# Performance work log

Measured on AMD Instinct MI355X. Metric: run time of the kernel, lower is better.

The kernel has to match this reference:

```python
import jax, jax.numpy as jnp
import numpy as np

HIDDEN = 384
NDIM = 3
N_POINTS = 100000
N_SUPER = 2048
MAX_DEG = 32
RADIUS = 0.045
INPUT_DIM = 3


def _sincos_embed(coords):
    # ContinuousSincosEmbed: dim=384, ndim=3 -> 128 channels per spatial dim (64 sin + 64 cos)
    eff = HIDDEN // NDIM  # 128
    omega = jnp.arange(0, eff, 2, dtype=jnp.float32) / eff
    freq = 1.0 / (10000.0 ** omega)  # [eff//2]
    out = coords[..., None] * freq  # [..., ndim, eff//2]
    emb = jnp.concatenate([jnp.sin(out), jnp.cos(out)], axis=-1)  # [..., ndim, eff]
    return emb.reshape(coords.shape[:-1] + (HIDDEN,))


def _radius_neighbors(pos, sn_idx):
    # numpy preprocessing equivalent of torch_geometric.nn.pool.radius with
    # max_num_neighbors=MAX_DEG; fixed-size padded [S, K] output + validity mask.
    nbr = np.zeros((N_SUPER, MAX_DEG), np.int32)
    mask = np.zeros((N_SUPER, MAX_DEG), bool)
    pos2 = (pos ** 2).sum(-1)
    r2 = RADIUS * RADIUS
    chunk = 128
    for i0 in range(0, N_SUPER, chunk):
        sp = pos[sn_idx[i0:i0 + chunk]]
        d2 = (sp ** 2).sum(-1)[:, None] + pos2[None, :] - 2.0 * (sp @ pos.T)
        within = d2 <= r2
        for j in range(sp.shape[0]):
            idx = np.nonzero(within[j])[0][:MAX_DEG]
            nbr[i0 + j, :len(idx)] = idx
            mask[i0 + j, :len(idx)] = True
    return nbr, mask


def setup_inputs() -> dict:
    rng = np.random.default_rng(0)
    pos = rng.random((N_POINTS, NDIM)).astype(np.float32)
    sn_idx = np.sort(rng.choice(N_POINTS, N_SUPER, replace=False)).astype(np.int32)
    nbr, mask = _radius_neighbors(pos, sn_idx)
    key = jax.random.key(0)
    ks = jax.random.split(key, 6)
    s = 0.02  # truncnormal002 init scale
    return {
        "input_pos": jnp.asarray(pos),
        "input_feat": jax.random.normal(ks[0], (N_POINTS, INPUT_DIM), jnp.float32),
        "supernode_idx": jnp.asarray(sn_idx),
        "neighbor_idx": jnp.asarray(nbr),
        "neighbor_mask": jnp.asarray(mask),
        "W_in": jax.random.normal(ks[1], (INPUT_DIM, HIDDEN), jnp.float32) * s,
        "b_in": jnp.zeros((HIDDEN,), jnp.float32),
        "W1": jax.random.normal(ks[2], (2 * HIDDEN, HIDDEN), jnp.float32) * s,
        "b1": jnp.zeros((HIDDEN,), jnp.float32),
        "W2": jax.random.normal(ks[3], (HIDDEN, HIDDEN), jnp.float32) * s,
        "b2": jnp.zeros((HIDDEN,), jnp.float32),
        "W_proj": jax.random.normal(ks[4], (2 * HIDDEN, HIDDEN), jnp.float32) * s,
        "b_proj": jnp.zeros((HIDDEN,), jnp.float32),
    }


def reference(input_pos, input_feat, supernode_idx, neighbor_idx, neighbor_mask,
              W_in, b_in, W1, b1, W2, b2, W_proj, b_proj):
    # point embeddings: continuous sincos pos embed + input feature projection
    x = _sincos_embed(input_pos) + input_feat @ W_in + b_in          # [N, D]
    sn = x[supernode_idx]                                            # [S, D] supernode pos embed
    src = x[neighbor_idx]                                            # [S, K, D] gathered neighbors
    dst = jnp.broadcast_to(sn[:, None, :], src.shape)                # [S, K, D]
    h = jnp.concatenate([src, dst], axis=-1)                         # [S, K, 2D]
    # message MLP (Linear -> GELU(exact) -> Linear), as nn.GELU default
    h = jax.nn.gelu(h @ W1 + b1, approximate=False) @ W2 + b2        # [S, K, D]
    # masked mean == segment_csr(..., reduce='mean') over variable-degree edges
    m = neighbor_mask[..., None].astype(h.dtype)
    agg = (h * m).sum(axis=1) / jnp.maximum(m.sum(axis=1), 1.0)      # [S, D]
    # readd_supernode_pos: concat supernode pos embed, project 2D -> D
    out = jnp.concatenate([agg, sn], axis=-1) @ W_proj + b_proj      # [S, D]
    return out[None]                                                 # [1, S, D] (batch_size=1)
```

## Files before the change

### kernel.cpp

```cpp
#include <hip/hip_runtime.h>
#include <hip/hip_bf16.h>
#include <cstdint>

#define HIDDEN 384
#define NSUPER 2048
#define FRAGS (12*24*64)
#define WBLK  (FRAGS*8)

typedef __attribute__((ext_vector_type(8))) short bf16x8;
typedef __attribute__((ext_vector_type(4))) float f32x4;

__device__ inline unsigned short f2bf(float f) {
    unsigned int u = __float_as_uint(f);
    return (unsigned short)((u + 0x7fffu + ((u >> 16) & 1u)) >> 16);
}
__device__ inline bf16x8 pack8(const float* v) {
    union { bf16x8 v8; unsigned short u[8]; } u;
    #pragma unroll
    for (int i = 0; i < 8; ++i) u.u[i] = f2bf(v[i]);
    return u.v8;
}
__device__ inline float gelu(float y) {
    const float y2 = y * y;
    const float m  = __expf(y * fmaf(-0.0713548163f, y2, -1.5957691216f));
    return y * (1.0f / (1.0f + m));
}

__global__ __launch_bounds__(256)
void prep(const float* __restrict__ W1, const float* __restrict__ W2,
          const float* __restrict__ Wp, const unsigned int* __restrict__ mask,
          const float* __restrict__ pos, const float* __restrict__ feat,
          const int* __restrict__ sn_idx,
          const float* __restrict__ W_in, const float* __restrict__ b_in,
          unsigned short* __restrict__ w1sf, unsigned short* __restrict__ w1df,
          unsigned short* __restrict__ w2f,  unsigned short* __restrict__ wpf,
          unsigned short* __restrict__ snxb, int* __restrict__ flag) {
    const int b = blockIdx.x;
    const int t = threadIdx.x;
    if (b == 360) {
        __shared__ int s;
        if (t == 0) s = 0;
        __syncthreads();
        int bad = 0;
        for (int i = t; i < 16384; i += 256)
            if (mask[i] > 1u) bad = 1;
        if (bad) s = 1;
        __syncthreads();
        if (t == 0) *flag = s;
        return;
    }
    if (b > 360) {
        __shared__ float W4[HIDDEN][4];
        __shared__ float P6[64][7];
        const int eb = b - 361;
        if (t < 64) {
            const int pi = sn_idx[eb*64 + t];
            P6[t][0]=pos[pi*3];  P6[t][1]=pos[pi*3+1];  P6[t][2]=pos[pi*3+2];
            P6[t][3]=feat[pi*3]; P6[t][4]=feat[pi*3+1]; P6[t][5]=feat[pi*3+2];
        }
        for (int d = t; d < HIDDEN; d += 256) {
            W4[d][0]=W_in[d]; W4[d][1]=W_in[HIDDEN+d];
            W4[d][2]=W_in[2*HIDDEN+d]; W4[d][3]=b_in[d];
        }
        __syncthreads();
        const int er = t >> 2, seg = t & 3;
        float frA[8], frB[8];
        #pragma unroll
        for (int i = 0; i < 8; ++i) {
            frA[i] = exp2f(-(float)(seg*8 + i)      * 0.2076205059304601f);
            frB[i] = exp2f(-(float)(32 + seg*8 + i) * 0.2076205059304601f);
        }
        const float f0 = P6[er][3], f1 = P6[er][4], f2 = P6[er][5];
        #pragma unroll
        for (int cc = 0; cc < 3; ++cc) {
            const float pc = P6[er][cc];
            float sL[8], sH[8], cL[8], cH[8];
            #pragma unroll
            for (int i = 0; i < 8; ++i) {
                const float aL = pc*frA[i], aH = pc*frB[i];
                sL[i]=__sinf(aL); sH[i]=__sinf(aH); cL[i]=__cosf(aL); cH[i]=__cosf(aH);
            }
            #pragma unroll
            for (int q = 0; q < 4; ++q) {
                const float* bb = (q==0)?sL:(q==1)?sH:(q==2)?cL:cH;
                const int blk = cc*4 + q;
                float v[8];
                #pragma unroll
                for (int i = 0; i < 8; ++i) {
                    const int dim = blk*32 + seg*8 + i;
                    const float4 wv = *(const float4*)W4[dim];
                    v[i] = fmaf(f0, wv.x, fmaf(f1, wv.y, fmaf(f2, wv.z, bb[i] + wv.w)));
                }
                *(bf16x8*)&snxb[(size_t)(eb*64 + er)*HIDDEN + blk*32 + seg*8] = pack8(v);
            }
        }
        return;
    }
    const int grp = b / 72, sub = b % 72;
    const float* W; unsigned short* out;
    switch (grp) {
        case 0: W = W1;              out = w1sf; break;
        case 1: W = W1 + 384*HIDDEN; out = w1df; break;
        case 2: W = W2;              out = w2f;  break;
        case 3: W = Wp;              out = wpf;  break;
        default:W = Wp + 384*HIDDEN; out = wpf + WBLK; break;
    }
    const int idx = sub * 256 + t;
    const int l   = idx & 63;
    const int frag= idx >> 6;
    const int nt  = frag % 24;
    const int kt  = frag / 24;
    const int col = nt * 16 + (l & 15);
    const int k0  = kt * 32 + (l >> 4) * 8;
    unsigned int pk[4];
    #pragma unroll
    for (int j = 0; j < 4; ++j) {
        unsigned int lo = f2bf(W[(size_t)(k0 + 2*j)     * HIDDEN + col]);
        unsigned int hi = f2bf(W[(size_t)(k0 + 2*j + 1) * HIDDEN + col]);
        pk[j] = lo | (hi << 16);
    }
    *reinterpret_cast<uint4*>(&out[(size_t)idx * 8]) =
        *reinterpret_cast<const uint4*>(pk);
}

__global__ __launch_bounds__(256)
void k_dstv(const unsigned short* __restrict__ snxb,
            const unsigned short* __restrict__ w1df,
            const float* __restrict__ b1, float* __restrict__ dstv) {
    const int rg = blockIdx.x >> 2, cq = blockIdx.x & 3;
    const int t = threadIdx.x, w = t>>6, l = t&63, lg = l>>4, l15 = l&15;
    const int wgm = w>>1, wgn = w&1;
    const int r0 = rg*64 + wgm*32;
    const int ntb = cq*6 + wgn*3;
    f32x4 acc[2][3];
    #pragma unroll
    for (int mt=0; mt<2; ++mt)
        #pragma unroll
        for (int nt=0; nt<3; ++nt) acc[mt][nt] = (f32x4){0.f,0.f,0.f,0.f};
    #pragma unroll 2
    for (int kt = 0; kt < 12; ++kt) {
        bf16x8 a[2], bfr[3];
        const unsigned short* bpp = &w1df[((size_t)(kt*24 + ntb)*64 + l)*8];
        #pragma unroll
        for (int nt=0; nt<3; ++nt) bfr[nt] = *(const bf16x8*)(bpp + (size_t)nt*512);
        #pragma unroll
        for (int mt=0; mt<2; ++mt)
            a[mt] = *(const bf16x8*)&snxb[(size_t)(r0 + mt*16 + l15)*HIDDEN + kt*32 + lg*8];
        #pragma unroll
        for (int mt=0; mt<2; ++mt)
            #pragma unroll
            for (int nt=0; nt<3; ++nt)
                acc[mt][nt] = __builtin_amdgcn_mfma_f32_16x16x32_bf16(a[mt], bfr[nt], acc[mt][nt], 0,0,0);
    }
    #pragma unroll
    for (int mt=0; mt<2; ++mt)
        #pragma unroll
        for (int nt=0; nt<3; ++nt) {
            const int col = cq*96 + wgn*48 + nt*16 + l15;
            #pragma unroll
            for (int r=0; r<4; ++r) {
                const int row = r0 + mt*16 + lg*4 + r;
                dstv[(size_t)row*HIDDEN + col] = acc[mt][nt][r] + b1[col];
            }
        }
}

__global__ __launch_bounds__(512, 2)
void k_mlp(const float* __restrict__ pos, const float* __restrict__ feat,
           const int* __restrict__ nbr_idx, const void* __restrict__ mask_raw,
           const int* __restrict__ mask_fmt,
           const float* __restrict__ W_in, const float* __restrict__ b_in,
           const float* __restrict__ dstv,
           const unsigned short* __restrict__ W1sf,
           unsigned short* __restrict__ aggpre, float* __restrict__ cntf)
{
    __shared__ unsigned short G[8*12*64*8];
    __shared__ ushort4 WINTB[HIDDEN];
    __shared__ float PF[128][7];
    __shared__ float CNT[4];

    const int t  = threadIdx.x;
    const int bm = blockIdx.x;
    const int l = t & 63, w = t >> 6;
    const int mg = w >> 2, ng = w & 3;
    const int lg = l >> 4, l15 = l & 15;

    float dvreg[2][6];
    #pragma unroll
    for (int sl = 0; sl < 2; ++sl)
        #pragma unroll
        for (int nt = 0; nt < 6; ++nt)
            dvreg[sl][nt] = dstv[(size_t)(bm*4 + mg*2 + sl)*HIDDEN + ng*96 + nt*16 + l15];

    if (t < 128) {
        const int e  = bm*128 + t;
        const int pi = nbr_idx[e];
        PF[t][0]=pos[pi*3];  PF[t][1]=pos[pi*3+1];  PF[t][2]=pos[pi*3+2];
        PF[t][3]=feat[pi*3]; PF[t][4]=feat[pi*3+1]; PF[t][5]=feat[pi*3+2];
        const int fmt = *mask_fmt;
        const int mv  = fmt ? (int)((const unsigned char*)mask_raw)[e]
                            : ((const int*)mask_raw)[e];
        PF[t][6] = mv ? 1.0f : 0.0f;
    }
    if (t >= 128 && t < 128 + HIDDEN) {
        const int d = t - 128;
        ushort4 wv;
        wv.x = f2bf(W_in[d]); wv.y = f2bf(W_in[HIDDEN+d]);
        wv.z = f2bf(W_in[2*HIDDEN+d]); wv.w = f2bf(b_in[d]);
        WINTB[d] = wv;
    }
    __syncthreads();
    if (t < 4) {
        float c = 0.f;
        for (int s = 0; s < 32; ++s) c += PF[t*32+s][6];
        CNT[t] = c;
    }

    {
        const int er = t >> 2, seg = t & 3;
        float frA[8], frB[8];
        #pragma unroll
        for (int i = 0; i < 8; ++i) {
            frA[i] = exp2f(-(float)(seg*8 + i)      * 0.2076205059304601f);
            frB[i] = exp2f(-(float)(32 + seg*8 + i) * 0.2076205059304601f);
        }
        const float f0 = PF[er][3], f1 = PF[er][4], f2 = PF[er][5];
        const float pc0 = PF[er][0], pc1 = PF[er][1], pc2 = PF[er][2];
        const int slotbase = (er>>4)*12*64 + seg*16 + (er&15);
        #pragma unroll
        for (int kt = 0; kt < 12; ++kt) {
            const float pc = (kt>>2)==0 ? pc0 : ((kt>>2)==1 ? pc1 : pc2);
            float v[8];
            #pragma unroll
            for (int i = 0; i < 8; ++i) {
                const float fr = (kt&1) ? frB[i] : frA[i];
                const float aa = pc * fr;
                const float base = ((kt>>1)&1) ? __cosf(aa) : __sinf(aa);
                const ushort4 wv = WINTB[kt*32 + seg*8 + i];
                v[i] = fmaf(__uint_as_float((unsigned)wv.x<<16), f0,
                       fmaf(__uint_as_float((unsigned)wv.y<<16), f1,
                       fmaf(__uint_as_float((unsigned)wv.z<<16), f2,
                            base + __uint_as_float((unsigned)wv.w<<16))));
            }
            *(bf16x8*)&G[(size_t)(slotbase + kt*64)*8] = pack8(v);
        }
    }
    __syncthreads();

    f32x4 acc[4][6];
    #pragma unroll
    for (int mt=0; mt<4; ++mt)
        #pragma unroll
        for (int nt=0; nt<6; ++nt) acc[mt][nt] = (f32x4){0.f,0.f,0.f,0.f};

    bf16x8 bA[6], bB[6];
    #define LOADB(dst, kt)                                                      \
        { const unsigned short* bp_ = &W1sf[((size_t)((kt)*24 + ng*6)*64 + l)*8];\
          _Pragma("unroll")                                                     \
          for (int nt_ = 0; nt_ < 6; ++nt_)                                     \
              dst[nt_] = *(const bf16x8*)(bp_ + (size_t)nt_*512); }
    #define AREAD(a_, kt)                                                       \
        { _Pragma("unroll")                                                     \
          for (int mt_ = 0; mt_ < 4; ++mt_)                                     \
              a_[mt_] = *(const bf16x8*)&G[(size_t)((((mg*4 + mt_)*12 + (kt))*64) + l)*8]; }
    #define MFMA6(bfr, a_)                                                      \
        { __builtin_amdgcn_s_setprio(1);                                        \
          _Pragma("unroll")                                                     \
          for (int mt_ = 0; mt_ < 4; ++mt_)                                     \
              _Pragma("unroll")                                                 \
              for (int nt_ = 0; nt_ < 6; ++nt_)                                 \
                  acc[mt_][nt_] = __builtin_amdgcn_mfma_f32_16x16x32_bf16(      \
                      a_[mt_], bfr[nt_], acc[mt_][nt_], 0, 0, 0);               \
          __builtin_amdgcn_s_setprio(0); }

    LOADB(bA, 0); LOADB(bB, 1);
    #pragma unroll
    for (int kt = 0; kt < 12; kt += 2) {
        bf16x8 a[4];
        AREAD(a, kt);
        MFMA6(bA, a);
        if (kt + 2 < 12) LOADB(bA, kt + 2);
        AREAD(a, kt + 1);
        MFMA6(bB, a);
        if (kt + 3 < 12) LOADB(bB, kt + 3);
    }

    float mvr[4][4];
    #pragma unroll
    for (int mt=0; mt<4; ++mt)
        #pragma unroll
        for (int r=0; r<4; ++r)
            mvr[mt][r] = PF[(mg*4 + mt)*16 + lg*4 + r][6];
    #pragma unroll
    for (int nt=0; nt<6; ++nt) {
        const int col = ng*96 + nt*16 + l15;
        float s0 = 0.f, s1 = 0.f;
        #pragma unroll
        for (int mt=0; mt<4; ++mt) {
            const float dv = dvreg[mt>>1][nt];
            float p = 0.f;
            #pragma unroll
            for (int r=0; r<4; ++r)
                p += mvr[mt][r] * gelu(acc[mt][nt][r] + dv);
            if (mt < 2) s0 += p; else s1 += p;
        }
        s0 += __shfl_xor(s0,16); s0 += __shfl_xor(s0,32);
        s1 += __shfl_xor(s1,16); s1 += __shfl_xor(s1,32);
        if (lg == 0) {
            const int sn0 = bm*4 + mg*2;
            aggpre[(size_t)sn0*HIDDEN + col]     = f2bf(s0 / fmaxf(CNT[mg*2],1.f));
            aggpre[(size_t)(sn0+1)*HIDDEN + col] = f2bf(s1 / fmaxf(CNT[mg*2+1],1.f));
        }
    }
    if (t < 4) cntf[bm*4 + t] = CNT[t];
    #undef LOADB
    #undef AREAD
    #undef MFMA6
}

__global__ __launch_bounds__(256)
void k_agg(const unsigned short* __restrict__ aggpre,
           const unsigned short* __restrict__ w2f,
           const float* __restrict__ b2, const float* __restrict__ cntf,
           unsigned short* __restrict__ aggb) {
    const int rg = blockIdx.x >> 2, cq = blockIdx.x & 3;
    const int t = threadIdx.x, w = t>>6, l = t&63, lg = l>>4, l15 = l&15;
    const int wgm = w>>1, wgn = w&1;
    const int r0 = rg*64 + wgm*32;
    const int ntb = cq*6 + wgn*3;
    f32x4 acc[2][3];
    #pragma unroll
    for (int mt=0; mt<2; ++mt)
        #pragma unroll
        for (int nt=0; nt<3; ++nt) acc[mt][nt] = (f32x4){0.f,0.f,0.f,0.f};
    #pragma unroll 2
    for (int kt = 0; kt < 12; ++kt) {
        bf16x8 a[2], bfr[3];
        const unsigned short* bpp = &w2f[((size_t)(kt*24 + ntb)*64 + l)*8];
        #pragma unroll
        for (int nt=0; nt<3; ++nt) bfr[nt] = *(const bf16x8*)(bpp + (size_t)nt*512);
        #pragma unroll
        for (int mt=0; mt<2; ++mt)
            a[mt] = *(const bf16x8*)&aggpre[(size_t)(r0 + mt*16 + l15)*HIDDEN + kt*32 + lg*8];
        #pragma unroll
        for (int mt=0; mt<2; ++mt)
            #pragma unroll
            for (int nt=0; nt<3; ++nt)
                acc[mt][nt] = __builtin_amdgcn_mfma_f32_16x16x32_bf16(a[mt], bfr[nt], acc[mt][nt], 0,0,0);
    }
    #pragma unroll
    for (int mt=0; mt<2; ++mt)
        #pragma unroll
        for (int nt=0; nt<3; ++nt) {
            const int col = cq*96 + wgn*48 + nt*16 + l15;
            const float bb = b2[col];
            #pragma unroll
            for (int r=0; r<4; ++r) {
                const int row = r0 + mt*16 + lg*4 + r;
                const float nz = (cntf[row] > 0.f) ? 1.f : 0.f;
                aggb[(size_t)row*HIDDEN + col] = f2bf(acc[mt][nt][r] + bb*nz);
            }
        }
}

__global__ __launch_bounds__(256)
void k_proj(const unsigned short* __restrict__ aggb,
            const unsigned short* __restrict__ snxb,
            const unsigned short* __restrict__ wpf,
            const float* __restrict__ bp, float* __restrict__ out) {
    const int rg = blockIdx.x >> 2, cq = blockIdx.x & 3;
    const int t = threadIdx.x, w = t>>6, l = t&63, lg = l>>4, l15 = l&15;
    const int wgm = w>>1, wgn = w&1;
    const int r0 = rg*64 + wgm*32;
    const int ntb = cq*6 + wgn*3;
    f32x4 acc[2][3];
    #pragma unroll
    for (int mt=0; mt<2; ++mt)
        #pragma unroll
        for (int nt=0; nt<3; ++nt) acc[mt][nt] = (f32x4){0.f,0.f,0.f,0.f};
    #pragma unroll 2
    for (int kt = 0; kt < 24; ++kt) {
        const unsigned short* Ab = (kt < 12) ? aggb : snxb;
        const unsigned short* Wb = (kt < 12) ? wpf  : wpf + WBLK;
        const int ktt = (kt < 12) ? kt : kt - 12;
        bf16x8 a[2], bfr[3];
        const unsigned short* bpp = &Wb[((size_t)(ktt*24 + ntb)*64 + l)*8];
        #pragma unroll
        for (int nt=0; nt<3; ++nt) bfr[nt] = *(const bf16x8*)(bpp + (size_t)nt*512);
        #pragma unroll
        for (int mt=0; mt<2; ++mt)
            a[mt] = *(const bf16x8*)&Ab[(size_t)(r0 + mt*16 + l15)*HIDDEN + ktt*32 + lg*8];
        #pragma unroll
        for (int mt=0; mt<2; ++mt)
            #pragma unroll
            for (int nt=0; nt<3; ++nt)
                acc[mt][nt] = __builtin_amdgcn_mfma_f32_16x16x32_bf16(a[mt], bfr[nt], acc[mt][nt], 0,0,0);
    }
    #pragma unroll
    for (int mt=0; mt<2; ++mt)
        #pragma unroll
        for (int nt=0; nt<3; ++nt) {
            const int col = cq*96 + wgn*48 + nt*16 + l15;
            #pragma unroll
            for (int r=0; r<4; ++r) {
                const int row = r0 + mt*16 + lg*4 + r;
                out[(size_t)row*HIDDEN + col] = acc[mt][nt][r] + bp[col];
            }
        }
}

extern "C" void kernel_launch(void* const* d_in, const int* in_sizes, int n_in,
                              void* d_out, int out_size, void* d_ws, size_t ws_size,
                              hipStream_t stream) {
    const float* pos   = (const float*)d_in[0];
    const float* feat  = (const float*)d_in[1];
    const int*   sn    = (const int*)d_in[2];
    const int*   nbr   = (const int*)d_in[3];
    const void*  mask  = d_in[4];
    const float* W_in  = (const float*)d_in[5];
    const float* b_in  = (const float*)d_in[6];
    const float* W1    = (const float*)d_in[7];
    const float* b1    = (const float*)d_in[8];
    const float* W2    = (const float*)d_in[9];
    const float* b2    = (const float*)d_in[10];
    const float* Wp    = (const float*)d_in[11];
    const float* bpv   = (const float*)d_in[12];
    float* out = (float*)d_out;

    char* base = (char*)d_ws;
    int* flag = (int*)base;
    unsigned short* w1sf = (unsigned short*)(base + 256);
    unsigned short* w1df = w1sf + WBLK;
    unsigned short* w2f  = w1df + WBLK;
    unsigned short* wpf  = w2f  + WBLK;
    unsigned short* snxb = wpf  + 2*(size_t)WBLK;
    unsigned short* aggb = snxb + (size_t)NSUPER*HIDDEN;
    unsigned short* aggp = aggb + (size_t)NSUPER*HIDDEN;
    float* cntf = (float*)(aggp + (size_t)NSUPER*HIDDEN);
    float* dstv = cntf + NSUPER;

    hipLaunchKernelGGL(prep, dim3(393), dim3(256), 0, stream,
                       W1, W2, Wp, (const unsigned int*)mask,
                       pos, feat, sn, W_in, b_in,
                       w1sf, w1df, w2f, wpf, snxb, flag);
    hipLaunchKernelGGL(k_dstv, dim3(128), dim3(256), 0, stream,
                       snxb, w1df, b1, dstv);
    hipLaunchKernelGGL(k_mlp, dim3(512), dim3(512), 0, stream,
                       pos, feat, nbr, mask, flag, W_in, b_in, dstv,
                       w1sf, aggp, cntf);
    hipLaunchKernelGGL(k_agg, dim3(128), dim3(256), 0, stream,
                       aggp, w2f, b2, cntf, aggb);
    hipLaunchKernelGGL(k_proj, dim3(128), dim3(256), 0, stream,
                       aggb, snxb, wpf, bpv, out);
}
```

Measured before the change: 87.21 us.

## Fuse W2 aggregation GEMM into projection kernel via shared-memory tile

Merges the k_agg and k_proj kernels into one k_out kernel. Each block computes the full 64x384 W2 output for its row group into shared memory, then runs the projection GEMM from that tile, removing one launch and the aggb global round trip. In exchange, each of the four column-quarter blocks per row group recomputes the whole W2 GEMM (4x redundant work), and the accumulator array per wave grows to 24 tiles, which raises register pressure. Separately, the input-projection weights in k_mlp are now kept as fp32 float4 in shared memory instead of bf16-packed values.

```diff
diff --git a/kernel.cpp b/kernel.cpp
--- a/kernel.cpp
+++ b/kernel.cpp
@@ -175,7 +175,7 @@
            unsigned short* __restrict__ aggpre, float* __restrict__ cntf)
 {
     __shared__ unsigned short G[8*12*64*8];
-    __shared__ ushort4 WINTB[HIDDEN];
+    __shared__ float4 WINT[HIDDEN];
     __shared__ float PF[128][7];
     __shared__ float CNT[4];
 
@@ -204,10 +204,7 @@
     }
     if (t >= 128 && t < 128 + HIDDEN) {
         const int d = t - 128;
-        ushort4 wv;
-        wv.x = f2bf(W_in[d]); wv.y = f2bf(W_in[HIDDEN+d]);
-        wv.z = f2bf(W_in[2*HIDDEN+d]); wv.w = f2bf(b_in[d]);
-        WINTB[d] = wv;
+        WINT[d] = (float4){W_in[d], W_in[HIDDEN+d], W_in[2*HIDDEN+d], b_in[d]};
     }
     __syncthreads();
     if (t < 4) {
@@ -236,11 +233,8 @@
                 const float fr = (kt&1) ? frB[i] : frA[i];
                 const float aa = pc * fr;
                 const float base = ((kt>>1)&1) ? __cosf(aa) : __sinf(aa);
-                const ushort4 wv = WINTB[kt*32 + seg*8 + i];
-                v[i] = fmaf(__uint_as_float((unsigned)wv.x<<16), f0,
-                       fmaf(__uint_as_float((unsigned)wv.y<<16), f1,
-                       fmaf(__uint_as_float((unsigned)wv.z<<16), f2,
-                            base + __uint_as_float((unsigned)wv.w<<16))));
+                const float4 wv = WINT[kt*32 + seg*8 + i];
+                v[i] = fmaf(f0, wv.x, fmaf(f1, wv.y, fmaf(f2, wv.z, base + wv.w)));
             }
             *(bf16x8*)&G[(size_t)(slotbase + kt*64)*8] = pack8(v);
         }
@@ -319,59 +313,56 @@
 }
 
 __global__ __launch_bounds__(256)
-void k_agg(const unsigned short* __restrict__ aggpre,
+void k_out(const unsigned short* __restrict__ aggpre,
+           const unsigned short* __restrict__ snxb,
            const unsigned short* __restrict__ w2f,
-           const float* __restrict__ b2, const float* __restrict__ cntf,
-           unsigned short* __restrict__ aggb) {
+           const unsigned short* __restrict__ wpf,
+           const float* __restrict__ b2, const float* __restrict__ bp,
+           const float* __restrict__ cntf, float* __restrict__ out) {
+    __shared__ unsigned short AGG[64][392];
     const int rg = blockIdx.x >> 2, cq = blockIdx.x & 3;
     const int t = threadIdx.x, w = t>>6, l = t&63, lg = l>>4, l15 = l&15;
     const int wgm = w>>1, wgn = w&1;
-    const int r0 = rg*64 + wgm*32;
-    const int ntb = cq*6 + wgn*3;
-    f32x4 acc[2][3];
-    #pragma unroll
-    for (int mt=0; mt<2; ++mt)
-        #pragma unroll
-        for (int nt=0; nt<3; ++nt) acc[mt][nt] = (f32x4){0.f,0.f,0.f,0.f};
-    #pragma unroll 2
-    for (int kt = 0; kt < 12; ++kt) {
-        bf16x8 a[2], bfr[3];
-        const unsigned short* bpp = &w2f[((size_t)(kt*24 + ntb)*64 + l)*8];
-        #pragma unroll
-        for (int nt=0; nt<3; ++nt) bfr[nt] = *(const bf16x8*)(bpp + (size_t)nt*512);
+    const int r0g = rg*64;
+
+    {
+        const int rowm = wgm*32;
+        f32x4 acc[2][12];
         #pragma unroll
         for (int mt=0; mt<2; ++mt)
-            a[mt] = *(const bf16x8*)&aggpre[(size_t)(r0 + mt*16 + l15)*HIDDEN + kt*32 + lg*8];
+            #pragma unroll
+            for (int nt=0; nt<12; ++nt) acc[mt][nt] = (f32x4){0.f,0.f,0.f,0.f};
+        for (int kt = 0; kt < 12; ++kt) {
+            bf16x8 a[2], bfr[12];
+            const unsigned short* bpp = &w2f[((size_t)(kt*24 + wgn*12)*64 + l)*8];
+            #pragma unroll
+            for (int nt=0; nt<12; ++nt) bfr[nt] = *(const bf16x8*)(bpp + (size_t)nt*512);
+            #pragma unroll
+            for (int mt=0; mt<2; ++mt)
+                a[mt] = *(const bf16x8*)&aggpre[(size_t)(r0g + rowm + mt*16 + l15)*HIDDEN + kt*32 + lg*8];
+            #pragma unroll
+            for (int mt=0; mt<2; ++mt)
+                #pragma unroll
+                for (int nt=0; nt<12; ++nt)
+                    acc[mt][nt] = __builtin_amdgcn_mfma_f32_16x16x32_bf16(a[mt], bfr[nt], acc[mt][nt], 0,0,0);
+        }
         #pragma unroll
         for (int mt=0; mt<2; ++mt)
             #pragma unroll
-            for (int nt=0; nt<3; ++nt)
-                acc[mt][nt] = __builtin_amdgcn_mfma_f32_16x16x32_bf16(a[mt], bfr[nt], acc[mt][nt], 0,0,0);
-    }
-    #pragma unroll
-    for (int mt=0; mt<2; ++mt)
-        #pragma unroll
-        for (int nt=0; nt<3; ++nt) {
-            const int col = cq*96 + wgn*48 + nt*16 + l15;
-            const float bb = b2[col];
-            #pragma unroll
-            for (int r=0; r<4; ++r) {
-                const int row = r0 + mt*16 + lg*4 + r;
-                const float nz = (cntf[row] > 0.f) ? 1.f : 0.f;
-                aggb[(size_t)row*HIDDEN + col] = f2bf(acc[mt][nt][r] + bb*nz);
-            }
-        }
-}
-
-__global__ __launch_bounds__(256)
-void k_proj(const unsigned short* __restrict__ aggb,
-            const unsigned short* __restrict__ snxb,
-            const unsigned short* __restrict__ wpf,
-            const float* __restrict__ bp, float* __restrict__ out) {
-    const int rg = blockIdx.x >> 2, cq = blockIdx.x & 3;
-    const int t = threadIdx.x, w = t>>6, l = t&63, lg = l>>4, l15 = l&15;
-    const int wgm = w>>1, wgn = w&1;
-    const int r0 = rg*64 + wgm*32;
+            for (int nt=0; nt<12; ++nt) {
+                const int col = wgn*192 + nt*16 + l15;
+                const float bb = b2[col];
+                #pragma unroll
+                for (int r=0; r<4; ++r) {
+                    const int row = rowm + mt*16 + lg*4 + r;
+                    const float nz = (cntf[r0g + row] > 0.f) ? 1.f : 0.f;
+                    AGG[row][col] = f2bf(acc[mt][nt][r] + bb*nz);
+                }
+            }
+    }
+    __syncthreads();
+
+    const int r0 = r0g + wgm*32;
     const int ntb = cq*6 + wgn*3;
     f32x4 acc[2][3];
     #pragma unroll
@@ -380,16 +371,19 @@
         for (int nt=0; nt<3; ++nt) acc[mt][nt] = (f32x4){0.f,0.f,0.f,0.f};
     #pragma unroll 2
     for (int kt = 0; kt < 24; ++kt) {
-        const unsigned short* Ab = (kt < 12) ? aggb : snxb;
-        const unsigned short* Wb = (kt < 12) ? wpf  : wpf + WBLK;
+        const unsigned short* Wb = (kt < 12) ? wpf : wpf + WBLK;
         const int ktt = (kt < 12) ? kt : kt - 12;
         bf16x8 a[2], bfr[3];
         const unsigned short* bpp = &Wb[((size_t)(ktt*24 + ntb)*64 + l)*8];
         #pragma unroll
         for (int nt=0; nt<3; ++nt) bfr[nt] = *(const bf16x8*)(bpp + (size_t)nt*512);
         #pragma unroll
-        for (int mt=0; mt<2; ++mt)
-            a[mt] = *(const bf16x8*)&Ab[(size_t)(r0 + mt*16 + l15)*HIDDEN + ktt*32 + lg*8];
+        for (int mt=0; mt<2; ++mt) {
+            if (kt < 12)
+                a[mt] = *(const bf16x8*)&AGG[wgm*32 + mt*16 + l15][ktt*32 + lg*8];
+            else
+                a[mt] = *(const bf16x8*)&snxb[(size_t)(r0 + mt*16 + l15)*HIDDEN + ktt*32 + lg*8];
+        }
         #pragma unroll
         for (int mt=0; mt<2; ++mt)
             #pragma unroll
@@ -434,8 +428,7 @@
     unsigned short* w2f  = w1df + WBLK;
     unsigned short* wpf  = w2f  + WBLK;
     unsigned short* snxb = wpf  + 2*(size_t)WBLK;
-    unsigned short* aggb = snxb + (size_t)NSUPER*HIDDEN;
-    unsigned short* aggp = aggb + (size_t)NSUPER*HIDDEN;
+    unsigned short* aggp = snxb + (size_t)NSUPER*HIDDEN;
     float* cntf = (float*)(aggp + (size_t)NSUPER*HIDDEN);
     float* dstv = cntf + NSUPER;
 
@@ -448,8 +441,6 @@
     hipLaunchKernelGGL(k_mlp, dim3(512), dim3(512), 0, stream,
                        pos, feat, nbr, mask, flag, W_in, b_in, dstv,
                        w1sf, aggp, cntf);
-    hipLaunchKernelGGL(k_agg, dim3(128), dim3(256), 0, stream,
-                       aggp, w2f, b2, cntf, aggb);
-    hipLaunchKernelGGL(k_proj, dim3(128), dim3(256), 0, stream,
-                       aggb, snxb, wpf, bpv, out);
-}
+    hipLaunchKernelGGL(k_out, dim3(128), dim3(256), 0, stream,
+                       aggp, snxb, w2f, wpf, b2, bpv, cntf, out);
+}
```

Result: slower. 89.62 us (+2.8%).
